# Performance work log

Hardware: AMD Instinct MI355X
Metric: run time of the kernel (lower is better)

## Reference

```python
import jax, jax.numpy as jnp
import numpy as np

HEADS = 4
KS = 7  # neighborhood window size


def group_norm(x, g, b, eps=1e-5):
    # GroupNorm(1, C) on NCHW: normalize over (C,H,W) per sample
    mu = x.mean(axis=(1, 2, 3), keepdims=True)
    var = x.var(axis=(1, 2, 3), keepdims=True)
    xn = (x - mu) * jax.lax.rsqrt(var + eps)
    return xn * g[None, :, None, None] + b[None, :, None, None]


def layer_norm(x, g, b, eps=1e-5):
    mu = x.mean(axis=-1, keepdims=True)
    var = x.var(axis=-1, keepdims=True)
    return (x - mu) * jax.lax.rsqrt(var + eps) * g + b


def na2d(x, qkv_w, qkv_b, proj_w, proj_b, rpb):
    # Neighborhood attention 2D (NATTEN semantics: window clamped at borders)
    N, H, W, C = x.shape
    e, k = HEADS, KS
    d = C // e
    qkv = x @ qkv_w.T + qkv_b  # [N,H,W,3C]
    q, kk, v = jnp.split(qkv, 3, axis=-1)
    q = q.reshape(N, H, W, e, d) * (d ** -0.5)
    kk = kk.reshape(N, H, W, e, d)
    v = v.reshape(N, H, W, e, d)
    ni = jnp.clip(jnp.arange(H) - k // 2, 0, H - k)[:, None] + jnp.arange(k)  # [H,k]
    nj = jnp.clip(jnp.arange(W) - k // 2, 0, W - k)[:, None] + jnp.arange(k)  # [W,k]
    kg = kk[:, ni][:, :, :, nj]  # [N,H,i,W,j,e,d]
    vg = v[:, ni][:, :, :, nj]
    scores = jnp.einsum('nhwed,nhiwjed->nhweij', q, kg)  # [N,H,W,e,k,k]
    ri = ni - jnp.arange(H)[:, None] + (k - 1)  # rel pos index in [0, 2k-2]
    rj = nj - jnp.arange(W)[:, None] + (k - 1)
    bias = rpb[:, ri][:, :, :, rj]  # [e,H,i,W,j]
    scores = scores + bias.transpose(1, 3, 0, 2, 4)[None]
    attn = jax.nn.softmax(scores.reshape(N, H, W, e, k * k), axis=-1).reshape(N, H, W, e, k, k)
    out = jnp.einsum('nhweij,nhiwjed->nhwed', attn, vg).reshape(N, H, W, C)
    return out @ proj_w.T + proj_b


def na_layer(x, gn_g, gn_b, qkv_w, qkv_b, proj_w, proj_b, rpb, ln_g, ln_b, fc1_w, fc1_b, fc2_w, fc2_b):
    N, C, H, W = x.shape
    x1 = x.transpose(0, 2, 3, 1)  # n h w c (pre-norm residual)
    xg = group_norm(x, gn_g, gn_b).transpose(0, 2, 3, 1)
    a = na2d(xg, qkv_w, qkv_b, proj_w, proj_b, rpb) + x1
    t = a.reshape(N, H * W, C)
    h = jax.nn.gelu(layer_norm(t, ln_g, ln_b) @ fc1_w.T + fc1_b, approximate=False)
    t = t + (h @ fc2_w.T + fc2_b)
    return t.reshape(N, H, W, C).transpose(0, 3, 1, 2)


def conv3x3(x, w, b):
    y = jax.lax.conv_general_dilated(x, w, (1, 1), 'SAME', dimension_numbers=('NCHW', 'OIHW', 'NCHW'))
    return y + b[None, :, None, None]


def setup_inputs() -> dict:
    key = jax.random.key(0)
    ks = jax.random.split(key, 16)
    N, C, H, W = 2, 128, 64, 64
    L, e, k, hid, red = 2, HEADS, KS, 4 * 128, 18
    rn = lambda kk, shape, s=0.02: jax.random.normal(kk, shape, jnp.float32) * s
    return {
        'x': jax.random.normal(ks[0], (N, C, H, W), jnp.float32),
        'gn_g': jnp.ones((L, C), jnp.float32), 'gn_b': jnp.zeros((L, C), jnp.float32),
        'qkv_w': rn(ks[1], (L, 3 * C, C)), 'qkv_b': jnp.zeros((L, 3 * C), jnp.float32),
        'proj_w': rn(ks[2], (L, C, C)), 'proj_b': jnp.zeros((L, C), jnp.float32),
        'rpb': rn(ks[3], (L, e, 2 * k - 1, 2 * k - 1)),
        'ln_g': jnp.ones((L, C), jnp.float32), 'ln_b': jnp.zeros((L, C), jnp.float32),
        'fc1_w': rn(ks[4], (L, hid, C)), 'fc1_b': jnp.zeros((L, hid), jnp.float32),
        'fc2_w': rn(ks[5], (L, C, hid)), 'fc2_b': jnp.zeros((L, C), jnp.float32),
        'bconv_w': rn(ks[6], (C, C, 3, 3)), 'bconv_b': jnp.zeros((C,), jnp.float32),
        'c1_w': rn(ks[7], (C // 4, C)), 'c1_b': jnp.zeros((C // 4,), jnp.float32),
        'c2_w': rn(ks[8], (C, C // 4)), 'c2_b': jnp.zeros((C,), jnp.float32),
        'ca1_w': rn(ks[9], (C // red, C)), 'ca1_b': jnp.zeros((C // red,), jnp.float32),
        'ca2_w': rn(ks[10], (C, C // red)), 'ca2_b': jnp.zeros((C,), jnp.float32),
    }


def reference(x, gn_g, gn_b, qkv_w, qkv_b, proj_w, proj_b, rpb, ln_g, ln_b, fc1_w, fc1_b, fc2_w, fc2_b, bconv_w, bconv_b, c1_w, c1_b, c2_w, c2_b, ca1_w, ca1_b, ca2_w, ca2_b):
    res = x
    for l in range(gn_g.shape[0]):  # n_resblocks (structurally fixed, small)
        res = na_layer(res, gn_g[l], gn_b[l], qkv_w[l], qkv_b[l], proj_w[l], proj_b[l], rpb[l],
                       ln_g[l], ln_b[l], fc1_w[l], fc1_b[l], fc2_w[l], fc2_b[l])
    res = conv3x3(res, bconv_w, bconv_b)
    # tail: 1x1 conv -> ReLU -> 1x1 conv -> CALayer
    y = jax.nn.relu(jnp.einsum('rc,nchw->nrhw', c1_w, res) + c1_b[None, :, None, None])
    y = jnp.einsum('cr,nrhw->nchw', c2_w, y) + c2_b[None, :, None, None]
    p = y.mean(axis=(2, 3))  # global avg pool -> [N,C]
    s = jax.nn.sigmoid(jax.nn.relu(p @ ca1_w.T + ca1_b) @ ca2_w.T + ca2_b)
    y = y * s[:, :, None, None]
    return y + x
```

## Files before the change

kernel.cpp:

```cpp
#include <hip/hip_runtime.h>
#include <math.h>

typedef unsigned short u16;

#define NN 2
#define CC 128
#define HH 64
#define WW 64
#define NHD 4
#define DH 32
#define KSZ 7
#define PIX (NN*HH*WW)
#define HID 512
#define C4 32
#define CRED 7
#define RW 22
#define RNB 160
#define NBV 154

typedef float f32x4 __attribute__((ext_vector_type(4)));
typedef short bf16x8 __attribute__((ext_vector_type(8)));

static __device__ __forceinline__ float u2f(u16 u){ return __uint_as_float(((unsigned)u) << 16); }
static __device__ __forceinline__ u16 f2u(float f){
    unsigned b = __float_as_uint(f);
    return (u16)((b + 0x7FFFu + ((b >> 16) & 1u)) >> 16);
}

__global__ void detect_k(const u16* __restrict__ x, int* __restrict__ flag,
                         float* __restrict__ poolacc){
    __shared__ float red[256];
    int t = threadIdx.x;
    float mx = 0.f;
    for(int i = t; i < 4096; i += 256){
        float v = fabsf(u2f(x[i]));
        if(v < 1e30f) mx = fmaxf(mx, v);
    }
    red[t] = mx; __syncthreads();
    for(int s = 128; s > 0; s >>= 1){
        if(t < s) red[t] = fmaxf(red[t], red[t+s]);
        __syncthreads();
    }
    if(t == 0) *flag = (red[0] > 1e6f) ? 1 : 0;
    if(t < NN*CC) poolacc[t] = 0.f;
}

struct PtrTab { const void* p[23]; int off[24]; };
#define NCVT 2172
#define NRPK 576
#define NNCH 512

__global__ __launch_bounds__(256) void setup_k(
    PtrTab tab, u16* __restrict__ Wb, u16* __restrict__ Wt,
    const void* __restrict__ convw, const void* __restrict__ x,
    float* __restrict__ cur, float* __restrict__ part,
    const int* __restrict__ flag, int total)
{
    int blk = blockIdx.x;
    int t = threadIdx.x;
    int fl = *flag;
    if(blk < NCVT){
        int i = blk*256 + t;
        if(i < total){
            int a = 0;
            while(i >= tab.off[a+1]) a++;
            int loc = i - tab.off[a];
            Wb[i] = fl ? f2u(((const float*)tab.p[a])[loc]) : ((const u16*)tab.p[a])[loc];
        }
        return;
    }
    if(blk < NCVT + NRPK){
        int i = (blk - NCVT)*256 + t;
        if(i < CC*CC*9){
            int o = i/(9*CC); int rem = i%(9*CC); int tap = rem/CC; int c = rem%CC;
            size_t s = (size_t)(o*CC + c)*9 + tap;
            Wt[i] = fl ? f2u(((const float*)convw)[s]) : ((const u16*)convw)[s];
        }
        return;
    }
    __shared__ float tile[32][65];
    __shared__ float wred[4][2];
    int u = blk - NCVT - NRPK;
    int bx = u & 3, by = u >> 2;
    int n = by >> 6, i = by & 63;
    for(int idx = t; idx < 32*64; idx += 256){
        int cl = idx >> 6, j = idx & 63;
        size_t src = ((size_t)(n*CC + bx*32 + cl)*HH + i)*WW + j;
        tile[cl][j] = fl ? ((const float*)x)[src] : u2f(((const u16*)x)[src]);
    }
    __syncthreads();
    float s = 0.f, q = 0.f;
    for(int idx = t; idx < 64*32; idx += 256){
        int j = idx >> 5, cl = idx & 31;
        float v = tile[cl][j];
        cur[((size_t)((n*HH + i)*WW) + j)*CC + bx*32 + cl] = v;
        s += v; q += v*v;
    }
    #pragma unroll
    for(int off = 32; off > 0; off >>= 1){ s += __shfl_xor(s, off, 64); q += __shfl_xor(q, off, 64); }
    int wave = t >> 6;
    if((t & 63) == 0){ wred[wave][0] = s; wred[wave][1] = q; }
    __syncthreads();
    if(t == 0){
        float ss = wred[0][0]+wred[1][0]+wred[2][0]+wred[3][0];
        float qq = wred[0][1]+wred[1][1]+wred[2][1]+wred[3][1];
        int pidx = n*256 + i*4 + bx;
        part[pidx*2] = ss; part[pidx*2+1] = qq;
    }
}

enum { EPI_NONE = 0, EPI_RES = 1, EPI_GELU = 2 };
enum { OUT_F32 = 0, OUT_BF16 = 1, OUT_BOTH = 2 };
enum { EX_NONE = 0, EX_STATS = 1 };
#define LDP 136

template<int EPI, int OUTM, int AGN, int EXTRA>
__global__ __launch_bounds__(256) void g64_k(
    const void* __restrict__ Av, const u16* __restrict__ W, const u16* __restrict__ bias,
    const float* __restrict__ R, float* __restrict__ Cf, u16* __restrict__ Cb,
    const u16* __restrict__ gnw, const u16* __restrict__ gnb,
    float* __restrict__ gnpart, int gncount,
    int M, int N, int K)
{
    __shared__ __align__(16) u16 As[64*LDP];
    __shared__ __align__(16) u16 Bs[64*LDP];
    __shared__ float wred[4][2];
    const int bm = blockIdx.y*64, bn = blockIdx.x*64;
    const int t = threadIdx.x;
    const int wave = t >> 6, lane = t & 63;
    const int wm = (wave >> 1)*32, wn = (wave & 1)*32;
    const int lg = lane >> 4, lr = lane & 15;
    const int nsm = bm >> 12;
    f32x4 acc[2][2];
    #pragma unroll
    for(int i = 0; i < 2; i++)
        #pragma unroll
        for(int j = 0; j < 2; j++) acc[i][j] = (f32x4){0.f,0.f,0.f,0.f};

    float gmu = 0.f, grs = 0.f;
    if(AGN){
        float a = 0.f, q = 0.f;
        for(int idx = lane; idx < gncount; idx += 64){
            a += gnpart[(nsm*gncount + idx)*2];
            q += gnpart[(nsm*gncount + idx)*2 + 1];
        }
        #pragma unroll
        for(int off = 32; off > 0; off >>= 1){
            a += __shfl_xor(a, off, 64); q += __shfl_xor(q, off, 64);
        }
        const float inv = 1.f/(float)(HH*WW*CC);
        gmu = a*inv;
        grs = rsqrtf(fmaxf(q*inv - gmu*gmu, 0.f) + 1e-5f);
    }

    for(int k0 = 0; k0 < K; k0 += 128){
        uint4 ra[4], rb[4];
        float4 fa[4][2];
        #pragma unroll
        for(int r = 0; r < 4; r++){
            int e = r*256 + t;
            int row = e >> 4, ch = e & 15;
            if(AGN){
                const float* ap = (const float*)Av + (size_t)(bm+row)*K + k0 + ch*8;
                fa[r][0] = *(const float4*)ap;
                fa[r][1] = *(const float4*)(ap + 4);
            } else {
                ra[r] = *(const uint4*)((const u16*)Av + (size_t)(bm+row)*K + k0 + ch*8);
            }
            rb[r] = (bn+row < N) ? *(const uint4*)(W + (size_t)(bn+row)*K + k0 + ch*8)
                                 : (uint4){0,0,0,0};
        }
        #pragma unroll
        for(int r = 0; r < 4; r++){
            int e = r*256 + t;
            int row = e >> 4, ch = e & 15;
            if(AGN){
                union { uint4 u; u16 h[8]; } g8, b8, o8;
                g8.u = *(const uint4*)(gnw + k0 + ch*8);
                b8.u = *(const uint4*)(gnb + k0 + ch*8);
                const float* fv = (const float*)&fa[r][0];
                #pragma unroll
                for(int z = 0; z < 8; z++)
                    o8.h[z] = f2u((fv[z]-gmu)*grs*u2f(g8.h[z]) + u2f(b8.h[z]));
                *(uint4*)&As[row*LDP + ch*8] = o8.u;
            } else {
                *(uint4*)&As[row*LDP + ch*8] = ra[r];
            }
            *(uint4*)&Bs[row*LDP + ch*8] = rb[r];
        }
        __syncthreads();
        #pragma unroll
        for(int kc = 0; kc < 4; kc++){
            bf16x8 af0 = *(const bf16x8*)&As[(wm + lr)*LDP      + kc*32 + lg*8];
            bf16x8 af1 = *(const bf16x8*)&As[(wm + 16 + lr)*LDP + kc*32 + lg*8];
            bf16x8 bf0 = *(const bf16x8*)&Bs[(wn + lr)*LDP      + kc*32 + lg*8];
            bf16x8 bf1 = *(const bf16x8*)&Bs[(wn + 16 + lr)*LDP + kc*32 + lg*8];
            acc[0][0] = __builtin_amdgcn_mfma_f32_16x16x32_bf16(af0, bf0, acc[0][0], 0, 0, 0);
            acc[0][1] = __builtin_amdgcn_mfma_f32_16x16x32_bf16(af0, bf1, acc[0][1], 0, 0, 0);
            acc[1][0] = __builtin_amdgcn_mfma_f32_16x16x32_bf16(af1, bf0, acc[1][0], 0, 0, 0);
            acc[1][1] = __builtin_amdgcn_mfma_f32_16x16x32_bf16(af1, bf1, acc[1][1], 0, 0, 0);
        }
        if(k0 + 128 < K) __syncthreads();
    }

    float ssum = 0.f, sq = 0.f;
    #pragma unroll
    for(int i = 0; i < 2; i++){
        #pragma unroll
        for(int j = 0; j < 2; j++){
            int col = bn + wn + j*16 + lr;
            if(col >= N) continue;
            #pragma unroll
            for(int reg = 0; reg < 4; reg++){
                int row = bm + wm + i*16 + lg*4 + reg;
                float v = acc[i][j][reg] + u2f(bias[col]);
                if(EPI == EPI_RES)  v += R[(size_t)row*N + col];
                if(EPI == EPI_GELU) v = 0.5f*v*(1.f + erff(v*0.70710678118f));
                if(OUTM == OUT_F32 || OUTM == OUT_BOTH) Cf[(size_t)row*N + col] = v;
                if(OUTM == OUT_BF16 || OUTM == OUT_BOTH) Cb[(size_t)row*N + col] = f2u(v);
                if(EXTRA == EX_STATS){ ssum += v; sq += v*v; }
            }
        }
    }
    if(EXTRA == EX_STATS){
        #pragma unroll
        for(int off = 32; off > 0; off >>= 1){
            ssum += __shfl_xor(ssum, off, 64); sq += __shfl_xor(sq, off, 64);
        }
        if(lane == 0){ wred[wave][0] = ssum; wred[wave][1] = sq; }
        __syncthreads();
        if(t == 0){
            int bidx = blockIdx.y*gridDim.x + blockIdx.x;
            gnpart[bidx*2]   = wred[0][0]+wred[1][0]+wred[2][0]+wred[3][0];
            gnpart[bidx*2+1] = wred[0][1]+wred[1][1]+wred[2][1]+wred[3][1];
        }
    }
}

__global__ __launch_bounds__(256) void proj_ln_k(
    const u16* __restrict__ A, const u16* __restrict__ W, const u16* __restrict__ bias,
    const float* __restrict__ R, const u16* __restrict__ lng, const u16* __restrict__ lnb,
    float* __restrict__ abuf, u16* __restrict__ lnout)
{
    __shared__ __align__(16) u16 As[32*LDP];
    __shared__ __align__(16) u16 Bs[128*LDP];
    __shared__ float redS[32][2], redQ[32][2], muS[32], rsS[32];
    const int bm = blockIdx.x*32;
    const int t = threadIdx.x;
    const int wave = t >> 6, lane = t & 63;
    const int wm = (wave >> 1)*16, wn = (wave & 1)*64;
    const int lg = lane >> 4, lr = lane & 15;

    {
        uint4 ra[2], rb[8];
        #pragma unroll
        for(int r = 0; r < 2; r++){
            int e = r*256 + t; int row = e >> 4, ch = e & 15;
            ra[r] = *(const uint4*)(A + (size_t)(bm+row)*CC + ch*8);
        }
        #pragma unroll
        for(int r = 0; r < 8; r++){
            int e = r*256 + t; int row = e >> 4, ch = e & 15;
            rb[r] = *(const uint4*)(W + (size_t)row*CC + ch*8);
        }
        #pragma unroll
        for(int r = 0; r < 2; r++){
            int e = r*256 + t; int row = e >> 4, ch = e & 15;
            *(uint4*)&As[row*LDP + ch*8] = ra[r];
        }
        #pragma unroll
        for(int r = 0; r < 8; r++){
            int e = r*256 + t; int row = e >> 4, ch = e & 15;
            *(uint4*)&Bs[row*LDP + ch*8] = rb[r];
        }
    }
    __syncthreads();

    f32x4 acc[4];
    #pragma unroll
    for(int j = 0; j < 4; j++) acc[j] = (f32x4){0.f,0.f,0.f,0.f};
    #pragma unroll
    for(int kc = 0; kc < 4; kc++){
        bf16x8 af = *(const bf16x8*)&As[(wm + lr)*LDP + kc*32 + lg*8];
        #pragma unroll
        for(int j = 0; j < 4; j++){
            bf16x8 bf = *(const bf16x8*)&Bs[(wn + j*16 + lr)*LDP + kc*32 + lg*8];
            acc[j] = __builtin_amdgcn_mfma_f32_16x16x32_bf16(af, bf, acc[j], 0, 0, 0);
        }
    }
    #pragma unroll
    for(int reg = 0; reg < 4; reg++){
        int rl = wm + lg*4 + reg;
        float rs_ = 0.f, rq_ = 0.f;
        #pragma unroll
        for(int j = 0; j < 4; j++){
            int col = wn + j*16 + lr;
            float v = acc[j][reg] + u2f(bias[col]) + R[(size_t)(bm+rl)*CC + col];
            acc[j][reg] = v;
            abuf[(size_t)(bm+rl)*CC + col] = v;
            rs_ += v; rq_ += v*v;
        }
        rs_ += __shfl_xor(rs_, 1, 64); rq_ += __shfl_xor(rq_, 1, 64);
        rs_ += __shfl_xor(rs_, 2, 64); rq_ += __shfl_xor(rq_, 2, 64);
        rs_ += __shfl_xor(rs_, 4, 64); rq_ += __shfl_xor(rq_, 4, 64);
        rs_ += __shfl_xor(rs_, 8, 64); rq_ += __shfl_xor(rq_, 8, 64);
        if(lr == 0){ redS[rl][wn>>6] = rs_; redQ[rl][wn>>6] = rq_; }
    }
    __syncthreads();
    if(t < 32){
        float mu = (redS[t][0] + redS[t][1])*(1.f/CC);
        float var = fmaxf((redQ[t][0] + redQ[t][1])*(1.f/CC) - mu*mu, 0.f);
        muS[t] = mu; rsS[t] = rsqrtf(var + 1e-5f);
    }
    __syncthreads();
    #pragma unroll
    for(int reg = 0; reg < 4; reg++){
        int rl = wm + lg*4 + reg;
        float mu = muS[rl], rstd = rsS[rl];
        #pragma unroll
        for(int j = 0; j < 4; j++){
            int col = wn + j*16 + lr;
            float v = (acc[j][reg] - mu)*rstd*u2f(lng[col]) + u2f(lnb[col]);
            lnout[(size_t)(bm+rl)*CC + col] = f2u(v);
        }
    }
}

__global__ __launch_bounds__(256) void mct_k(
    const u16* __restrict__ in, const u16* __restrict__ Wt, const u16* __restrict__ bias,
    const u16* __restrict__ c1w, const u16* __restrict__ c1b,
    const u16* __restrict__ c2w, const u16* __restrict__ c2b,
    float* __restrict__ ybuf, float* __restrict__ poolacc)
{
    __shared__ __align__(16) u16 As[32*LDP];
    __shared__ __align__(16) u16 Bs[128*LDP];
    u16* Bs1 = Bs;
    u16* Bs2 = Bs + 32*LDP;
    u16* Hs  = Bs + 32*LDP + 128*40;
    const int bm = blockIdx.x*32;
    const int t = threadIdx.x;
    const int wave = t >> 6, lane = t & 63;
    const int wm = (wave >> 1)*16, wn = (wave & 1)*64;
    const int lg = lane >> 4, lr = lane & 15;
    const int nsm = bm >> 12;

    uint4 rb1[2], rb2[2];
    #pragma unroll
    for(int r = 0; r < 2; r++){
        int e = r*256 + t; int row = e >> 4, ch = e & 15;
        rb1[r] = *(const uint4*)(c1w + (size_t)row*CC + ch*8);
    }
    #pragma unroll
    for(int r = 0; r < 2; r++){
        int e = r*256 + t; int row = e >> 2, ch = e & 3;
        rb2[r] = *(const uint4*)(c2w + (size_t)row*C4 + ch*8);
    }

    f32x4 acc[4];
    #pragma unroll
    for(int j = 0; j < 4; j++) acc[j] = (f32x4){0.f,0.f,0.f,0.f};

    for(int tap = 0; tap < 9; tap++){
        int dy = tap/3 - 1, dx = tap%3 - 1;
        uint4 ra[2], rb[8];
        #pragma unroll
        for(int r = 0; r < 2; r++){
            int e = r*256 + t; int row = e >> 4, ch = e & 15;
            int p = bm + row;
            int n = p >> 12, ii = (p & 4095) >> 6, jj = p & 63;
            int y = ii + dy, x = jj + dx;
            ra[r] = (uint4){0,0,0,0};
            if(y >= 0 && y < HH && x >= 0 && x < WW)
                ra[r] = *(const uint4*)(in + (size_t)(((n*HH + y)*WW + x))*CC + ch*8);
        }
        #pragma unroll
        for(int r = 0; r < 8; r++){
            int e = r*256 + t; int row = e >> 4, ch = e & 15;
            rb[r] = *(const uint4*)(Wt + (size_t)row*(9*CC) + tap*128 + ch*8);
        }
        #pragma unroll
        for(int r = 0; r < 2; r++){
            int e = r*256 + t; int row = e >> 4, ch = e & 15;
            *(uint4*)&As[row*LDP + ch*8] = ra[r];
        }
        #pragma unroll
        for(int r = 0; r < 8; r++){
            int e = r*256 + t; int row = e >> 4, ch = e & 15;
            *(uint4*)&Bs[row*LDP + ch*8] = rb[r];
        }
        __syncthreads();
        #pragma unroll
        for(int kc = 0; kc < 4; kc++){
            bf16x8 af = *(const bf16x8*)&As[(wm + lr)*LDP + kc*32 + lg*8];
            #pragma unroll
            for(int j = 0; j < 4; j++){
                bf16x8 bf = *(const bf16x8*)&Bs[(wn + j*16 + lr)*LDP + kc*32 + lg*8];
                acc[j] = __builtin_amdgcn_mfma_f32_16x16x32_bf16(af, bf, acc[j], 0, 0, 0);
            }
        }
        __syncthreads();
    }

    #pragma unroll
    for(int j = 0; j < 4; j++){
        int col = wn + j*16 + lr;
        #pragma unroll
        for(int reg = 0; reg < 4; reg++){
            int rl = wm + lg*4 + reg;
            As[rl*LDP + col] = f2u(acc[j][reg] + u2f(bias[col]));
        }
    }
    #pragma unroll
    for(int r = 0; r < 2; r++){
        int e = r*256 + t; int row = e >> 4, ch = e & 15;
        *(uint4*)&Bs1[row*LDP + ch*8] = rb1[r];
    }
    #pragma unroll
    for(int r = 0; r < 2; r++){
        int e = r*256 + t; int row = e >> 2, ch = e & 3;
        *(uint4*)&Bs2[row*40 + ch*8] = rb2[r];
    }
    __syncthreads();

    {
        const int wn1 = (wave & 1)*16;
        f32x4 a1 = (f32x4){0.f,0.f,0.f,0.f};
        #pragma unroll
        for(int kc = 0; kc < 4; kc++){
            bf16x8 af = *(const bf16x8*)&As[(wm + lr)*LDP + kc*32 + lg*8];
            bf16x8 bf = *(const bf16x8*)&Bs1[(wn1 + lr)*LDP + kc*32 + lg*8];
            a1 = __builtin_amdgcn_mfma_f32_16x16x32_bf16(af, bf, a1, 0, 0, 0);
        }
        #pragma unroll
        for(int reg = 0; reg < 4; reg++){
            int rl = wm + lg*4 + reg;
            int col = wn1 + lr;
            Hs[rl*40 + col] = f2u(fmaxf(a1[reg] + u2f(c1b[col]), 0.f));
        }
    }
    __syncthreads();

    {
        f32x4 a2[4];
        #pragma unroll
        for(int j = 0; j < 4; j++) a2[j] = (f32x4){0.f,0.f,0.f,0.f};
        bf16x8 af = *(const bf16x8*)&Hs[(wm + lr)*40 + lg*8];
        #pragma unroll
        for(int j = 0; j < 4; j++){
            bf16x8 bf = *(const bf16x8*)&Bs2[(wn + j*16 + lr)*40 + lg*8];
            a2[j] = __builtin_amdgcn_mfma_f32_16x16x32_bf16(af, bf, a2[j], 0, 0, 0);
        }
        float cs[4] = {0.f,0.f,0.f,0.f};
        #pragma unroll
        for(int j = 0; j < 4; j++){
            int col = wn + j*16 + lr;
            #pragma unroll
            for(int reg = 0; reg < 4; reg++){
                int row = bm + wm + lg*4 + reg;
                float v = a2[j][reg] + u2f(c2b[col]);
                ybuf[(size_t)row*CC + col] = v;
                cs[j] += v;
            }
        }
        #pragma unroll
        for(int j = 0; j < 4; j++){
            cs[j] += __shfl_xor(cs[j], 16, 64);
            cs[j] += __shfl_xor(cs[j], 32, 64);
        }
        if(lg == 0){
            #pragma unroll
            for(int j = 0; j < 4; j++)
                atomicAdd(&poolacc[nsm*CC + wn + j*16 + lr], cs[j]);
        }
    }
}

#define KVP 72
#define PSP 168

__global__ __launch_bounds__(128) void att_tile_k(
    const u16* __restrict__ qkv, const u16* __restrict__ rpb, u16* __restrict__ out)
{
    __shared__ __align__(16) u16 KV[2][RNB][KVP];
    __shared__ __align__(16) u16 Qs[16][64];
    __shared__ float rpbs[2][169];
    u16* PsB = &KV[0][0][0];
    const int blk = blockIdx.x;
    const int rb = blk >> 1, eg = blk & 1;
    const int p0 = rb*16;
    const int jb = p0 & 63, i = (p0 >> 6) & 63, n = p0 >> 12;
    const int i0 = min(max(i-3, 0), HH-KSZ);
    const int rc0 = min(max(jb-3, 0), WW-KSZ);
    const int t = threadIdx.x;

    for(int idx = t; idx < 2*169; idx += 128)
        rpbs[idx/169][idx%169] = u2f(rpb[(eg*2 + idx/169)*169 + idx%169]);
    {
        int pix = t >> 3, ch = t & 7;
        *(uint4*)&Qs[pix][ch*8] = *(const uint4*)(qkv + (size_t)(p0+pix)*(3*CC) + eg*64 + ch*8);
    }
    for(int idx = t; idx < RNB*16; idx += 128){
        int nb = idx >> 4, part = idx & 15;
        int kv = part >> 3, ch = part & 7;
        uint4 v = (uint4){0,0,0,0};
        if(nb < NBV){
            int ky = nb/RW, kcol = nb - ky*RW;
            int sy = i0 + ky, sx = min(rc0 + kcol, WW-1);
            v = *(const uint4*)(qkv + (size_t)((n*HH + sy)*WW + sx)*(3*CC) + CC + kv*CC + eg*64 + ch*8);
        }
        *(uint4*)&KV[kv][nb][ch*8] = v;
    }
    __syncthreads();

    const int el = t >> 6;
    const int lane = t & 63, lg = lane >> 4, lr = lane & 15;

    bf16x8 aq = *(const bf16x8*)&Qs[lr][el*32 + lg*8];
    f32x4 sc[10];
    #pragma unroll
    for(int c = 0; c < 10; c++){
        bf16x8 bk = *(const bf16x8*)&KV[0][c*16+lr][el*32 + lg*8];
        sc[c] = __builtin_amdgcn_mfma_f32_16x16x32_bf16(aq, bk, (f32x4){0.f,0.f,0.f,0.f}, 0, 0, 0);
    }
    __syncthreads();
    #pragma unroll
    for(int reg = 0; reg < 4; reg++){
        int pix = lg*4 + reg;
        int j = jb + pix;
        int base = min(max(j-3, 0), WW-KSZ) - rc0;
        float mx = -1e30f;
        #pragma unroll
        for(int c = 0; c < 10; c++){
            int nb = c*16 + lr;
            int ky = nb/RW, kcol = nb - ky*RW;
            float v = -1e30f;
            if(nb < NBV && kcol >= base && kcol <= base+6){
                int ri = i0 + ky - i + (KSZ-1);
                int rj = rc0 + kcol - j + (KSZ-1);
                v = sc[c][reg]*0.17677669529663689f + rpbs[el][ri*13 + rj];
            }
            sc[c][reg] = v;
            mx = fmaxf(mx, v);
        }
        mx = fmaxf(mx, __shfl_xor(mx, 1, 64));
        mx = fmaxf(mx, __shfl_xor(mx, 2, 64));
        mx = fmaxf(mx, __shfl_xor(mx, 4, 64));
        mx = fmaxf(mx, __shfl_xor(mx, 8, 64));
        float sum = 0.f;
        #pragma unroll
        for(int c = 0; c < 10; c++){
            float p = __expf(sc[c][reg] - mx);
            sc[c][reg] = p; sum += p;
        }
        sum += __shfl_xor(sum, 1, 64);
        sum += __shfl_xor(sum, 2, 64);
        sum += __shfl_xor(sum, 4, 64);
        sum += __shfl_xor(sum, 8, 64);
        float rs = 1.f/sum;
        #pragma unroll
        for(int c = 0; c < 10; c++)
            PsB[(el*16 + pix)*PSP + c*16 + lr] = f2u(sc[c][reg]*rs);
    }
    __syncthreads();
    f32x4 o0 = (f32x4){0.f,0.f,0.f,0.f}, o1 = (f32x4){0.f,0.f,0.f,0.f};
    #pragma unroll
    for(int ks = 0; ks < 5; ks++){
        bf16x8 ap = *(const bf16x8*)&PsB[(el*16 + lr)*PSP + ks*32 + lg*8];
        bf16x8 b0, b1;
        #pragma unroll
        for(int jj = 0; jj < 8; jj++){
            int nb = ks*32 + lg*8 + jj;
            b0[jj] = (short)KV[1][nb][el*32 + lr];
            b1[jj] = (short)KV[1][nb][el*32 + 16 + lr];
        }
        o0 = __builtin_amdgcn_mfma_f32_16x16x32_bf16(ap, b0, o0, 0, 0, 0);
        o1 = __builtin_amdgcn_mfma_f32_16x16x32_bf16(ap, b1, o1, 0, 0, 0);
    }
    int e = eg*2 + el;
    #pragma unroll
    for(int reg = 0; reg < 4; reg++){
        int pix = lg*4 + reg;
        out[(size_t)(p0+pix)*CC + e*32 + lr]      = f2u(o0[reg]);
        out[(size_t)(p0+pix)*CC + e*32 + 16 + lr] = f2u(o1[reg]);
    }
}

__global__ __launch_bounds__(256) void final_ca_k(
    const float* __restrict__ y, const float* __restrict__ poolacc,
    const u16* __restrict__ w1, const u16* __restrict__ b1,
    const u16* __restrict__ w2, const u16* __restrict__ b2,
    const void* __restrict__ xraw, void* __restrict__ outv,
    const int* __restrict__ flag)
{
    __shared__ float t1s[CRED];
    __shared__ float sres;
    int id0 = blockIdx.x*256;
    int c = (id0 >> 12) & (CC-1);
    int n = id0 >> 19;
    int t = threadIdx.x;
    if(t < CRED){
        float a = u2f(b1[t]);
        const float pscale = 1.f/(float)(HH*WW);
        for(int cc = 0; cc < CC; cc++)
            a += poolacc[n*CC + cc]*pscale*u2f(w1[t*CC + cc]);
        t1s[t] = fmaxf(a, 0.f);
    }
    __syncthreads();
    if(t == 0){
        float a = u2f(b2[c]);
        #pragma unroll
        for(int r = 0; r < CRED; r++) a += t1s[r]*u2f(w2[c*CRED + r]);
        sres = 1.f/(1.f + __expf(-a));
    }
    __syncthreads();
    float s = sres;
    int id = id0 + t;
    int j = id & 63; int i = (id >> 6) & 63;
    float xr = (*flag) ? ((const float*)xraw)[id] : u2f(((const u16*)xraw)[id]);
    float v = y[(size_t)((n*HH + i)*WW + j)*CC + c]*s + xr;
    if(*flag) ((float*)outv)[id] = v;
    else      ((u16*)outv)[id] = f2u(v);
}

extern "C" void kernel_launch(void* const* d_in, const int* in_sizes, int n_in,
                              void* d_out, int out_size, void* d_ws, size_t ws_size,
                              hipStream_t stream){
    float* wsf    = (float*)d_ws;
    int*   flagp  = (int*)d_ws;
    float* gnpart = wsf + 8;
    float* poolacc= wsf + 1040;

    u16* Wb = (u16*)(wsf + 2048);
    static const int wsizes[23] = {256,256,98304,768,32768,256,1352,256,256,131072,1024,
                                   131072,256,147456,128,4096,32,4096,128,896,7,896,128};
    int woff[24]; woff[0] = 0;
    for(int i = 0; i < 23; i++) woff[i+1] = woff[i] + wsizes[i];
    const int WTOT = woff[23];
    u16* Wt = Wb + 555760;

    float* AB    = wsf + 360448;
    float* cur   = AB;
    u16*  cur16  = (u16*)(AB + 1048576);
    u16*  xg16   = (u16*)(AB + 1572864);
    u16*  qkv16  = (u16*)(AB + 2097152);
    float* abuf  = AB + 2097152;
    u16*  hbuf16 = (u16*)(AB + 3670016);
    float* ybuf  = AB + 3670016;

    detect_k<<<1, 256, 0, stream>>>((const u16*)d_in[0], flagp, poolacc);

    PtrTab tab;
    for(int i = 0; i < 23; i++){ tab.p[i] = d_in[i+1]; tab.off[i] = woff[i]; }
    tab.off[23] = woff[23];
    setup_k<<<NCVT + NRPK + NNCH, 256, 0, stream>>>(
        tab, Wb, Wt, d_in[14], d_in[0], cur, gnpart, flagp, WTOT);

    const u16 *gng = Wb+woff[0], *gnb = Wb+woff[1], *qkvw = Wb+woff[2], *qkvb = Wb+woff[3],
              *projw = Wb+woff[4], *projb = Wb+woff[5], *rpbw = Wb+woff[6], *lng = Wb+woff[7],
              *lnb = Wb+woff[8], *f1w = Wb+woff[9], *f1b = Wb+woff[10], *f2w = Wb+woff[11],
              *f2b = Wb+woff[12], *bcb = Wb+woff[14], *c1w = Wb+woff[15],
              *c1b = Wb+woff[16], *c2w = Wb+woff[17], *c2b = Wb+woff[18], *ca1w = Wb+woff[19],
              *ca1b = Wb+woff[20], *ca2w = Wb+woff[21], *ca2b = Wb+woff[22];

    for(int l = 0; l < 2; l++){
        int gncount = (l == 0) ? 256 : 128;

        g64_k<EPI_NONE,OUT_BF16,1,EX_NONE><<<dim3(6, PIX/64), 256, 0, stream>>>(
            cur, qkvw + (size_t)l*3*CC*CC, qkvb + l*3*CC, nullptr, nullptr, qkv16,
            gng + l*CC, gnb + l*CC, gnpart, gncount, PIX, 3*CC, CC);

        att_tile_k<<<PIX/16*2, 128, 0, stream>>>(qkv16, rpbw + l*NHD*169, xg16);

        proj_ln_k<<<PIX/32, 256, 0, stream>>>(
            xg16, projw + (size_t)l*CC*CC, projb + l*CC, cur, lng + l*CC, lnb + l*CC,
            abuf, xg16);

        g64_k<EPI_GELU,OUT_BF16,0,EX_NONE><<<dim3(8, PIX/64), 256, 0, stream>>>(
            xg16, f1w + (size_t)l*HID*CC, f1b + l*HID, nullptr, nullptr, hbuf16,
            nullptr, nullptr, nullptr, 0, PIX, HID, CC);

        g64_k<EPI_RES,OUT_BOTH,0,EX_STATS><<<dim3(2, PIX/64), 256, 0, stream>>>(
            hbuf16, f2w + (size_t)l*CC*HID, f2b + l*CC, abuf, cur, cur16,
            nullptr, nullptr, gnpart, 0, PIX, CC, HID);
    }

    mct_k<<<PIX/32, 256, 0, stream>>>(cur16, Wt, bcb, c1w, c1b, c2w, c2b, ybuf, poolacc);

    final_ca_k<<<(NN*CC*HH*WW)/256, 256, 0, stream>>>(
        ybuf, poolacc, ca1w, ca1b, ca2w, ca2b, d_in[0], d_out, flagp);
}
```

Before: 271.8 us.

## Fuse projection, LayerNorm, MLP and GroupNorm stats into one kernel

Replaces the proj+LN kernel and the two MLP GEMM launches with a single mlp_k that handles 16 rows per block. The GELU hidden activations stay in shared memory, and the residual is kept in registers. This removes the global round-trips for the hidden buffer and the intermediate residual buffer, along with two launches. In exchange, every block reloads the full proj, fc1 and fc2 weights in chunks with many barriers, and the small 16-row tiles raise L2 weight traffic and give less MFMA work per block. Residual buffers now ping-pong between two fp32 arrays.

```diff
diff --git a/kernel.cpp b/kernel.cpp
--- a/kernel.cpp
+++ b/kernel.cpp
@@ -237,92 +237,175 @@
     }
 }
 
-__global__ __launch_bounds__(256) void proj_ln_k(
-    const u16* __restrict__ A, const u16* __restrict__ W, const u16* __restrict__ bias,
-    const float* __restrict__ R, const u16* __restrict__ lng, const u16* __restrict__ lnb,
-    float* __restrict__ abuf, u16* __restrict__ lnout)
+#define HSP 520
+
+__global__ __launch_bounds__(256) void mlp_k(
+    const u16* __restrict__ A,
+    const float* __restrict__ curin,
+    const u16* __restrict__ projw, const u16* __restrict__ projb,
+    const u16* __restrict__ lng, const u16* __restrict__ lnb,
+    const u16* __restrict__ f1w, const u16* __restrict__ f1b,
+    const u16* __restrict__ f2w, const u16* __restrict__ f2b,
+    float* __restrict__ curout, u16* __restrict__ cur16,
+    float* __restrict__ gnpart)
 {
-    __shared__ __align__(16) u16 As[32*LDP];
+    __shared__ __align__(16) u16 As[16*LDP];
+    __shared__ __align__(16) u16 Ls[16*LDP];
     __shared__ __align__(16) u16 Bs[128*LDP];
-    __shared__ float redS[32][2], redQ[32][2], muS[32], rsS[32];
-    const int bm = blockIdx.x*32;
+    __shared__ __align__(16) u16 Hs[16*HSP];
+    __shared__ float redS[16][4], redQ[16][4], muS[16], rsS[16];
+    __shared__ float wred[4][2];
+    const int bm = blockIdx.x*16;
     const int t = threadIdx.x;
     const int wave = t >> 6, lane = t & 63;
-    const int wm = (wave >> 1)*16, wn = (wave & 1)*64;
+    const int wn = wave*32;
     const int lg = lane >> 4, lr = lane & 15;
+    const int nsm = bm >> 12;
 
     {
-        uint4 ra[2], rb[8];
-        #pragma unroll
-        for(int r = 0; r < 2; r++){
-            int e = r*256 + t; int row = e >> 4, ch = e & 15;
-            ra[r] = *(const uint4*)(A + (size_t)(bm+row)*CC + ch*8);
-        }
+        int row = t >> 4, ch = t & 15;
+        uint4 ra = *(const uint4*)(A + (size_t)(bm+row)*CC + ch*8);
+        uint4 rb[8];
         #pragma unroll
         for(int r = 0; r < 8; r++){
-            int e = r*256 + t; int row = e >> 4, ch = e & 15;
-            rb[r] = *(const uint4*)(W + (size_t)row*CC + ch*8);
-        }
-        #pragma unroll
-        for(int r = 0; r < 2; r++){
-            int e = r*256 + t; int row = e >> 4, ch = e & 15;
-            *(uint4*)&As[row*LDP + ch*8] = ra[r];
-        }
+            int e = r*256 + t; int rw = e >> 4, c2 = e & 15;
+            rb[r] = *(const uint4*)(projw + (size_t)rw*CC + c2*8);
+        }
+        *(uint4*)&As[row*LDP + ch*8] = ra;
         #pragma unroll
         for(int r = 0; r < 8; r++){
-            int e = r*256 + t; int row = e >> 4, ch = e & 15;
-            *(uint4*)&Bs[row*LDP + ch*8] = rb[r];
-        }
-    }
-    __syncthreads();
-
-    f32x4 acc[4];
-    #pragma unroll
-    for(int j = 0; j < 4; j++) acc[j] = (f32x4){0.f,0.f,0.f,0.f};
+            int e = r*256 + t; int rw = e >> 4, c2 = e & 15;
+            *(uint4*)&Bs[rw*LDP + c2*8] = rb[r];
+        }
+    }
+    __syncthreads();
+
+    f32x4 acc[2];
+    acc[0] = (f32x4){0.f,0.f,0.f,0.f}; acc[1] = (f32x4){0.f,0.f,0.f,0.f};
     #pragma unroll
     for(int kc = 0; kc < 4; kc++){
-        bf16x8 af = *(const bf16x8*)&As[(wm + lr)*LDP + kc*32 + lg*8];
-        #pragma unroll
-        for(int j = 0; j < 4; j++){
+        bf16x8 af = *(const bf16x8*)&As[lr*LDP + kc*32 + lg*8];
+        #pragma unroll
+        for(int j = 0; j < 2; j++){
             bf16x8 bf = *(const bf16x8*)&Bs[(wn + j*16 + lr)*LDP + kc*32 + lg*8];
             acc[j] = __builtin_amdgcn_mfma_f32_16x16x32_bf16(af, bf, acc[j], 0, 0, 0);
         }
     }
+    float av[2][4];
     #pragma unroll
     for(int reg = 0; reg < 4; reg++){
-        int rl = wm + lg*4 + reg;
+        int rl = lg*4 + reg;
         float rs_ = 0.f, rq_ = 0.f;
         #pragma unroll
-        for(int j = 0; j < 4; j++){
+        for(int j = 0; j < 2; j++){
             int col = wn + j*16 + lr;
-            float v = acc[j][reg] + u2f(bias[col]) + R[(size_t)(bm+rl)*CC + col];
-            acc[j][reg] = v;
-            abuf[(size_t)(bm+rl)*CC + col] = v;
+            float v = acc[j][reg] + u2f(projb[col]) + curin[(size_t)(bm+rl)*CC + col];
+            av[j][reg] = v;
             rs_ += v; rq_ += v*v;
         }
         rs_ += __shfl_xor(rs_, 1, 64); rq_ += __shfl_xor(rq_, 1, 64);
         rs_ += __shfl_xor(rs_, 2, 64); rq_ += __shfl_xor(rq_, 2, 64);
         rs_ += __shfl_xor(rs_, 4, 64); rq_ += __shfl_xor(rq_, 4, 64);
         rs_ += __shfl_xor(rs_, 8, 64); rq_ += __shfl_xor(rq_, 8, 64);
-        if(lr == 0){ redS[rl][wn>>6] = rs_; redQ[rl][wn>>6] = rq_; }
-    }
-    __syncthreads();
-    if(t < 32){
-        float mu = (redS[t][0] + redS[t][1])*(1.f/CC);
-        float var = fmaxf((redQ[t][0] + redQ[t][1])*(1.f/CC) - mu*mu, 0.f);
+        if(lr == 0){ redS[rl][wave] = rs_; redQ[rl][wave] = rq_; }
+    }
+    __syncthreads();
+    if(t < 16){
+        float mu = (redS[t][0]+redS[t][1]+redS[t][2]+redS[t][3])*(1.f/CC);
+        float var = fmaxf((redQ[t][0]+redQ[t][1]+redQ[t][2]+redQ[t][3])*(1.f/CC) - mu*mu, 0.f);
         muS[t] = mu; rsS[t] = rsqrtf(var + 1e-5f);
     }
     __syncthreads();
     #pragma unroll
     for(int reg = 0; reg < 4; reg++){
-        int rl = wm + lg*4 + reg;
+        int rl = lg*4 + reg;
         float mu = muS[rl], rstd = rsS[rl];
         #pragma unroll
-        for(int j = 0; j < 4; j++){
+        for(int j = 0; j < 2; j++){
             int col = wn + j*16 + lr;
-            float v = (acc[j][reg] - mu)*rstd*u2f(lng[col]) + u2f(lnb[col]);
-            lnout[(size_t)(bm+rl)*CC + col] = f2u(v);
-        }
+            Ls[rl*LDP + col] = f2u((av[j][reg] - mu)*rstd*u2f(lng[col]) + u2f(lnb[col]));
+        }
+    }
+
+    for(int nc = 0; nc < 8; nc++){
+        uint4 rb[4];
+        #pragma unroll
+        for(int r = 0; r < 4; r++){
+            int e = r*256 + t; int rw = e >> 4, ch = e & 15;
+            rb[r] = *(const uint4*)(f1w + (size_t)(nc*64 + rw)*CC + ch*8);
+        }
+        __syncthreads();
+        #pragma unroll
+        for(int r = 0; r < 4; r++){
+            int e = r*256 + t; int rw = e >> 4, ch = e & 15;
+            *(uint4*)&Bs[rw*LDP + ch*8] = rb[r];
+        }
+        __syncthreads();
+        f32x4 a1 = (f32x4){0.f,0.f,0.f,0.f};
+        #pragma unroll
+        for(int kc = 0; kc < 4; kc++){
+            bf16x8 af = *(const bf16x8*)&Ls[lr*LDP + kc*32 + lg*8];
+            bf16x8 bf = *(const bf16x8*)&Bs[(wave*16 + lr)*LDP + kc*32 + lg*8];
+            a1 = __builtin_amdgcn_mfma_f32_16x16x32_bf16(af, bf, a1, 0, 0, 0);
+        }
+        #pragma unroll
+        for(int reg = 0; reg < 4; reg++){
+            int rl = lg*4 + reg;
+            int col = nc*64 + wave*16 + lr;
+            float v = a1[reg] + u2f(f1b[col]);
+            v = 0.5f*v*(1.f + erff(v*0.70710678118f));
+            Hs[rl*HSP + col] = f2u(v);
+        }
+    }
+
+    f32x4 a2[2];
+    a2[0] = (f32x4){0.f,0.f,0.f,0.f}; a2[1] = (f32x4){0.f,0.f,0.f,0.f};
+    for(int kc2 = 0; kc2 < 4; kc2++){
+        uint4 rb[8];
+        #pragma unroll
+        for(int r = 0; r < 8; r++){
+            int e = r*256 + t; int rw = e >> 4, ch = e & 15;
+            rb[r] = *(const uint4*)(f2w + (size_t)rw*HID + kc2*128 + ch*8);
+        }
+        __syncthreads();
+        #pragma unroll
+        for(int r = 0; r < 8; r++){
+            int e = r*256 + t; int rw = e >> 4, ch = e & 15;
+            *(uint4*)&Bs[rw*LDP + ch*8] = rb[r];
+        }
+        __syncthreads();
+        #pragma unroll
+        for(int kk = 0; kk < 4; kk++){
+            bf16x8 af = *(const bf16x8*)&Hs[lr*HSP + kc2*128 + kk*32 + lg*8];
+            #pragma unroll
+            for(int j = 0; j < 2; j++){
+                bf16x8 bf = *(const bf16x8*)&Bs[(wn + j*16 + lr)*LDP + kk*32 + lg*8];
+                a2[j] = __builtin_amdgcn_mfma_f32_16x16x32_bf16(af, bf, a2[j], 0, 0, 0);
+            }
+        }
+    }
+    float ssum = 0.f, sq = 0.f;
+    #pragma unroll
+    for(int j = 0; j < 2; j++){
+        int col = wn + j*16 + lr;
+        #pragma unroll
+        for(int reg = 0; reg < 4; reg++){
+            int row = bm + lg*4 + reg;
+            float v = a2[j][reg] + u2f(f2b[col]) + av[j][reg];
+            curout[(size_t)row*CC + col] = v;
+            cur16[(size_t)row*CC + col] = f2u(v);
+            ssum += v; sq += v*v;
+        }
+    }
+    #pragma unroll
+    for(int off = 32; off > 0; off >>= 1){
+        ssum += __shfl_xor(ssum, off, 64); sq += __shfl_xor(sq, off, 64);
+    }
+    if(lane == 0){ wred[wave][0] = ssum; wred[wave][1] = sq; }
+    __syncthreads();
+    if(t == 0){
+        gnpart[blockIdx.x*2]   = wred[0][0]+wred[1][0]+wred[2][0]+wred[3][0];
+        gnpart[blockIdx.x*2+1] = wred[0][1]+wred[1][1]+wred[2][1]+wred[3][1];
     }
 }
 
@@ -643,9 +726,8 @@
     u16*  cur16  = (u16*)(AB + 1048576);
     u16*  xg16   = (u16*)(AB + 1572864);
     u16*  qkv16  = (u16*)(AB + 2097152);
-    float* abuf  = AB + 2097152;
-    u16*  hbuf16 = (u16*)(AB + 3670016);
-    float* ybuf  = AB + 3670016;
+    float* cur2  = AB + 3670016;
+    float* ybuf  = AB + 2097152;
 
     detect_k<<<1, 256, 0, stream>>>((const u16*)d_in[0], flagp, poolacc);
 
@@ -662,26 +744,21 @@
               *c1b = Wb+woff[16], *c2w = Wb+woff[17], *c2b = Wb+woff[18], *ca1w = Wb+woff[19],
               *ca1b = Wb+woff[20], *ca2w = Wb+woff[21], *ca2b = Wb+woff[22];
 
+    float* rin = cur;
+    float* rout = cur2;
     for(int l = 0; l < 2; l++){
-        int gncount = (l == 0) ? 256 : 128;
-
         g64_k<EPI_NONE,OUT_BF16,1,EX_NONE><<<dim3(6, PIX/64), 256, 0, stream>>>(
-            cur, qkvw + (size_t)l*3*CC*CC, qkvb + l*3*CC, nullptr, nullptr, qkv16,
-            gng + l*CC, gnb + l*CC, gnpart, gncount, PIX, 3*CC, CC);
+            rin, qkvw + (size_t)l*3*CC*CC, qkvb + l*3*CC, nullptr, nullptr, qkv16,
+            gng + l*CC, gnb + l*CC, gnpart, 256, PIX, 3*CC, CC);
 
         att_tile_k<<<PIX/16*2, 128, 0, stream>>>(qkv16, rpbw + l*NHD*169, xg16);
 
-        proj_ln_k<<<PIX/32, 256, 0, stream>>>(
-            xg16, projw + (size_t)l*CC*CC, projb + l*CC, cur, lng + l*CC, lnb + l*CC,
-            abuf, xg16);
-
-        g64_k<EPI_GELU,OUT_BF16,0,EX_NONE><<<dim3(8, PIX/64), 256, 0, stream>>>(
-            xg16, f1w + (size_t)l*HID*CC, f1b + l*HID, nullptr, nullptr, hbuf16,
-            nullptr, nullptr, nullptr, 0, PIX, HID, CC);
-
-        g64_k<EPI_RES,OUT_BOTH,0,EX_STATS><<<dim3(2, PIX/64), 256, 0, stream>>>(
-            hbuf16, f2w + (size_t)l*CC*HID, f2b + l*CC, abuf, cur, cur16,
-            nullptr, nullptr, gnpart, 0, PIX, CC, HID);
+        mlp_k<<<PIX/16, 256, 0, stream>>>(
+            xg16, rin, projw + (size_t)l*CC*CC, projb + l*CC, lng + l*CC, lnb + l*CC,
+            f1w + (size_t)l*HID*CC, f1b + l*HID, f2w + (size_t)l*CC*HID, f2b + l*CC,
+            rout, cur16, gnpart);
+
+        float* tmp = rin; rin = rout; rout = tmp;
     }
 
     mct_k<<<PIX/32, 256, 0, stream>>>(cur16, Wt, bcb, c1w, c1b, c2w, c2b, ybuf, poolacc);
```

Result: slower. 355.9 us (+31.0%).
